# Optimization experiments

Hardware: AMD Instinct MI355X
Metric: run time of the kernel (lower is better)

## Reference

```python
import jax, jax.numpy as jnp
import numpy as np


def gcn_conv(x, edge_index, edge_weight, W, b):
    """PyG-style GCNConv: h = x @ W; add self-loops (w=1); sym deg^-1/2 norm;
    scatter-add aggregation; + bias."""
    N = x.shape[0]
    h = x @ W                                   # [N, F_out]
    row, col = edge_index[0], edge_index[1]     # src, dst
    loop = jnp.arange(N)
    row = jnp.concatenate([row, loop])
    col = jnp.concatenate([col, loop])
    ew = jnp.concatenate([edge_weight, jnp.ones((N,), edge_weight.dtype)])
    deg = jax.ops.segment_sum(ew, col, num_segments=N)
    dinv = jnp.where(deg > 0, deg ** -0.5, 0.0)
    norm = dinv[row] * ew * dinv[col]           # [E+N]
    out = jax.ops.segment_sum(h[row] * norm[:, None], col, num_segments=N)
    return out + b


def setup_inputs() -> dict:
    key = jax.random.key(0)
    ks = jax.random.split(key, 12)
    N, F_in, H, O, E = 20000, 3000, 512, 256, 640000
    x = jax.random.normal(ks[0], (N, F_in), dtype=jnp.float32)
    sim_edge_index = jax.random.randint(ks[1], (2, E), 0, N, dtype=jnp.int64)
    sim_edge_weight = jax.random.uniform(ks[2], (E,), dtype=jnp.float32)
    dist_edge_index = jax.random.randint(ks[3], (2, E), 0, N, dtype=jnp.int64)
    dist_edge_weight = jax.random.uniform(ks[4], (E,), dtype=jnp.float32)
    s = 0.02
    return {
        "x": x,
        "sim_edge_index": sim_edge_index,
        "sim_edge_weight": sim_edge_weight,
        "dist_edge_index": dist_edge_index,
        "dist_edge_weight": dist_edge_weight,
        "W1": jax.random.normal(ks[5], (F_in, H), dtype=jnp.float32) * s,
        "b1": jnp.zeros((H,), jnp.float32),
        "W2": jax.random.normal(ks[6], (F_in, H), dtype=jnp.float32) * s,
        "b2": jnp.zeros((H,), jnp.float32),
        "Ws": jax.random.normal(ks[7], (H, O), dtype=jnp.float32) * s,
        "bs": jnp.zeros((O,), jnp.float32),
        "Wd": jax.random.normal(ks[8], (H, O), dtype=jnp.float32) * s,
        "bd": jnp.zeros((O,), jnp.float32),
        "Wf": jax.random.normal(ks[9], (2 * O, O), dtype=jnp.float32) * s,
        "bf": jnp.zeros((O,), jnp.float32),
    }


def reference(x, sim_edge_index, sim_edge_weight, dist_edge_index,
              dist_edge_weight, W1, b1, W2, b2, Ws, bs, Wd, bd, Wf, bf):
    # eval mode: dropout is identity
    xs = jax.nn.relu(gcn_conv(x, sim_edge_index, sim_edge_weight, W1, b1))
    xd = jax.nn.relu(gcn_conv(x, dist_edge_index, dist_edge_weight, W2, b2))
    x_sim = gcn_conv(xs, sim_edge_index, sim_edge_weight, Ws, bs)
    x_dist = gcn_conv(xd, dist_edge_index, dist_edge_weight, Wd, bd)
    fused = jnp.concatenate([x_sim, x_dist], axis=1) @ Wf + bf
    return (x_sim, x_dist, fused)
```

## Files before the change

kernel.cpp:

```cpp
#include <hip/hip_runtime.h>
#include <cstdint>
#include <cstddef>

typedef unsigned short u16;
typedef __bf16 bf16x8 __attribute__((ext_vector_type(8)));
typedef float f32x4 __attribute__((ext_vector_type(4)));

#define N_NODES 20000
#define MPAD    20096
#define E_EDGES 640000
#define K1      3000
#define K1P     3008
#define H_DIM   512
#define NW      1024
#define O_DIM   256

__device__ __forceinline__ float bf2f(unsigned int hi) {
  union { unsigned int u; float f; } v; v.u = hi << 16; return v.f;
}
__device__ __forceinline__ u16 f2bf(float f) {
  union { float f; unsigned int u; } v; v.f = f;
  unsigned int u = v.u;
  return (u16)((u + 0x7fffu + ((u >> 16) & 1u)) >> 16);
}

__device__ __forceinline__ void gl2lds16(const void* g, void* l) {
  __builtin_amdgcn_global_load_lds((const __attribute__((address_space(1))) void*)g,
                                   (__attribute__((address_space(3))) void*)l, 16, 0, 0);
}

__global__ __launch_bounds__(256) void deg_init_k(float* degS, float* degD, int* cntS, int* cntD) {
  int i = blockIdx.x * 256 + threadIdx.x;
  if (i < N_NODES) { degS[i] = 1.0f; degD[i] = 1.0f; cntS[i] = 0; cntD[i] = 0; }
}

__global__ __launch_bounds__(256) void deg_accum_k(const int* eiS, const float* ewS,
                                                   const int* eiD, const float* ewD,
                                                   float* degS, float* degD, int* cntS, int* cntD) {
  int e = blockIdx.x * 256 + threadIdx.x;
  if (e < E_EDGES) {
    int cs = eiS[E_EDGES + e];
    atomicAdd(&degS[cs], ewS[e]);
    atomicAdd(&cntS[cs], 1);
    int cd = eiD[E_EDGES + e];
    atomicAdd(&degD[cd], ewD[e]);
    atomicAdd(&cntD[cd], 1);
  }
}

__global__ __launch_bounds__(256) void dinv_k(const float* degS, const float* degD,
                                              float* dinvS, float* dinvD) {
  int i = blockIdx.x * 256 + threadIdx.x;
  if (i < N_NODES) { dinvS[i] = rsqrtf(degS[i]); dinvD[i] = rsqrtf(degD[i]); }
}

__global__ __launch_bounds__(1024) void scan_k(const int* cntS, int* offS, int* curS,
                                               const int* cntD, int* offD, int* curD) {
  const int* cnt = blockIdx.x ? cntD : cntS;
  int* off = blockIdx.x ? offD : offS;
  int* cur = blockIdx.x ? curD : curS;
  __shared__ int sums[1024];
  const int t = threadIdx.x;
  const int CH = 20;
  int base = t * CH;
  int s = 0;
  for (int j = 0; j < CH; ++j) { int idx = base + j; if (idx < N_NODES) s += cnt[idx]; }
  sums[t] = s;
  __syncthreads();
  for (int d = 1; d < 1024; d <<= 1) {
    int v = (t >= d) ? sums[t - d] : 0;
    __syncthreads();
    sums[t] += v;
    __syncthreads();
  }
  int run = sums[t] - s;
  for (int j = 0; j < CH; ++j) {
    int idx = base + j;
    if (idx <= N_NODES) {
      off[idx] = run; cur[idx] = run;
      if (idx < N_NODES) run += cnt[idx];
    }
  }
}

__global__ __launch_bounds__(256) void scatter_k(const int* eiS, const float* ewS, const float* dinvS,
                                                 int* curS, int* ssrcS, float* snrmS,
                                                 const int* eiD, const float* ewD, const float* dinvD,
                                                 int* curD, int* ssrcD, float* snrmD) {
  int e = blockIdx.x * 256 + threadIdx.x;
  if (e < E_EDGES) {
    {
      int r = eiS[e], c = eiS[E_EDGES + e];
      int pos = atomicAdd(&curS[c], 1);
      ssrcS[pos] = r;
      snrmS[pos] = dinvS[r] * ewS[e] * dinvS[c];
    }
    {
      int r = eiD[e], c = eiD[E_EDGES + e];
      int pos = atomicAdd(&curD[c], 1);
      ssrcD[pos] = r;
      snrmD[pos] = dinvD[r] * ewD[e] * dinvD[c];
    }
  }
}

__global__ __launch_bounds__(256) void conv_x_k(const float* __restrict__ x, u16* __restrict__ xb) {
  const int row = blockIdx.x;
  for (int c = threadIdx.x; c < 376; c += 256) {
    uint4 o = {0, 0, 0, 0};
    if (row < N_NODES && c < 375) {
      const float4* p = (const float4*)(x + (size_t)row * K1 + (size_t)c * 8);
      float4 v0 = p[0], v1 = p[1];
      o.x = f2bf(v0.x) | ((unsigned)f2bf(v0.y) << 16);
      o.y = f2bf(v0.z) | ((unsigned)f2bf(v0.w) << 16);
      o.z = f2bf(v1.x) | ((unsigned)f2bf(v1.y) << 16);
      o.w = f2bf(v1.z) | ((unsigned)f2bf(v1.w) << 16);
    }
    *(uint4*)(xb + (size_t)row * K1P + (size_t)c * 8) = o;
  }
}

__global__ __launch_bounds__(256) void conv_w12_k(const float* __restrict__ W1,
                                                  const float* __restrict__ W2,
                                                  u16* __restrict__ w12t) {
  __shared__ float t[64][65];
  const int kb = blockIdx.x;
  const int nb = blockIdx.y;
  const int n0 = nb * 64;
  const float* W = (n0 < H_DIM) ? W1 : W2;
  const int nn0 = n0 & (H_DIM - 1);
  const int k0 = kb * 64;
  const int tc = threadIdx.x & 63;
  const int tr4 = threadIdx.x >> 6;
#pragma unroll
  for (int rr = 0; rr < 16; ++rr) {
    int r = tr4 * 16 + rr;
    int k = k0 + r;
    t[r][tc] = (k < K1) ? W[(size_t)k * H_DIM + nn0 + tc] : 0.f;
  }
  __syncthreads();
#pragma unroll
  for (int rr = 0; rr < 16; ++rr) {
    int n = tr4 * 16 + rr;
    w12t[(size_t)(n0 + n) * K1P + k0 + tc] = f2bf(t[tc][n]);
  }
}

__global__ __launch_bounds__(256) void conv_wsm_k(const float* Ws, const float* Wd, const float* Wf,
                                                  u16* wst, u16* wdt, u16* wft) {
  __shared__ float t[64][65];
  const int which = blockIdx.z;
  const float* W = (which == 0) ? Ws : (which == 1) ? Wd : Wf;
  u16* o = (which == 0) ? wst : (which == 1) ? wdt : wft;
  const int k0 = blockIdx.x * 64;
  const int n0 = blockIdx.y * 64;
  const int tc = threadIdx.x & 63;
  const int tr4 = threadIdx.x >> 6;
#pragma unroll
  for (int rr = 0; rr < 16; ++rr) {
    int r = tr4 * 16 + rr;
    t[r][tc] = W[(size_t)(k0 + r) * O_DIM + n0 + tc];
  }
  __syncthreads();
#pragma unroll
  for (int rr = 0; rr < 16; ++rr) {
    int n = tr4 * 16 + rr;
    o[(size_t)(n0 + n) * H_DIM + k0 + tc] = f2bf(t[tc][n]);
  }
}

template <typename CT, bool BIAS>
__device__ __forceinline__ void gemm_body(const u16* __restrict__ A, const u16* __restrict__ Bt,
                                          CT* __restrict__ C, const float* __restrict__ bias,
                                          int Mreal, int K, int ldc, int bm, int bn) {
  __shared__ alignas(16) u16 As[128 * 64];
  __shared__ alignas(16) u16 Bs[128 * 64];
  const int tid = threadIdx.x;
  const int lane = tid & 63;
  const int wv = tid >> 6;

  const int wm = (wv >> 1) << 6;
  const int wn = (wv & 1) << 6;
  const int frow = lane & 15;
  const int q = lane >> 4;
  const int r7 = lane & 7;

  const int srow = tid >> 3;
  const int sgr = ((tid & 7) ^ ((tid >> 3) & 7)) << 3;
  const u16* ga = A + (size_t)(bm + srow) * K + sgr;
  const u16* gb = Bt + (size_t)(bn + srow) * K + sgr;
  u16* la = &As[wv * 512];
  u16* lb = &Bs[wv * 512];

  f32x4 acc[4][4] = {};

  for (int k0 = 0; k0 < K; k0 += 64) {
#pragma unroll
    for (int r = 0; r < 4; ++r) {
      gl2lds16(ga + (size_t)(r * 32) * K + k0, la + r * 2048);
      gl2lds16(gb + (size_t)(r * 32) * K + k0, lb + r * 2048);
    }
    __syncthreads();
#pragma unroll
    for (int ks = 0; ks < 64; ks += 32) {
      const int p = (((q + (ks >> 3)) ^ r7) << 3);
      bf16x8 af[4], bv[4];
#pragma unroll
      for (int t = 0; t < 4; ++t) {
        af[t] = *(const bf16x8*)&As[(wm + t * 16 + frow) * 64 + p];
        bv[t] = *(const bf16x8*)&Bs[(wn + t * 16 + frow) * 64 + p];
      }
#pragma unroll
      for (int i = 0; i < 4; ++i)
#pragma unroll
        for (int j = 0; j < 4; ++j)
          acc[i][j] = __builtin_amdgcn_mfma_f32_16x16x32_bf16(af[i], bv[j], acc[i][j], 0, 0, 0);
    }
    __syncthreads();
  }

  const int crow = (lane >> 4) << 2;
  const int ccol = lane & 15;
#pragma unroll
  for (int i = 0; i < 4; ++i) {
#pragma unroll
    for (int r = 0; r < 4; ++r) {
      int gr = bm + wm + i * 16 + crow + r;
      if (gr < Mreal) {
#pragma unroll
        for (int j = 0; j < 4; ++j) {
          int gc = bn + wn + j * 16 + ccol;
          float v = acc[i][j][r];
          if constexpr (BIAS) v += bias[gc];
          if constexpr (sizeof(CT) == 2) C[(size_t)gr * ldc + gc] = (CT)f2bf(v);
          else C[(size_t)gr * ldc + gc] = (CT)v;
        }
      }
    }
  }
}

__global__ __launch_bounds__(256) void gemm_big_k(const u16* __restrict__ A,
                                                  const u16* __restrict__ Bt,
                                                  u16* __restrict__ C) {
  const int h = blockIdx.y * 8 + blockIdx.x;
  const int chunk = 157;
  const int L = (h & 7) * chunk + (h >> 3);
  const int bn = (L & 7) * 128;
  const int bm = (L >> 3) * 128;
  gemm_body<u16, false>(A, Bt, C, nullptr, N_NODES, K1P, NW, bm, bn);
}

__global__ __launch_bounds__(256) void gemm_pair_k(const u16* A0, const u16* B0, u16* C0,
                                                   const u16* A1, const u16* B1, u16* C1) {
  const u16* A = blockIdx.z ? A1 : A0;
  const u16* Bt = blockIdx.z ? B1 : B0;
  u16* C = blockIdx.z ? C1 : C0;
  gemm_body<u16, false>(A, Bt, C, nullptr, N_NODES, H_DIM, O_DIM,
                        blockIdx.y * 128, blockIdx.x * 128);
}

__global__ __launch_bounds__(256) void gemm_f_k(const u16* A, const u16* Bt, float* C,
                                                const float* bias) {
  gemm_body<float, true>(A, Bt, C, bias, N_NODES, H_DIM, O_DIM,
                         blockIdx.y * 128, blockIdx.x * 128);
}

__global__ __launch_bounds__(256) void agg1_k(const u16* __restrict__ h12,
                                              const int* offS, const int* srcS, const float* nrmS,
                                              const float* dinvS, const float* b1,
                                              const int* offD, const int* srcD, const float* nrmD,
                                              const float* dinvD, const float* b2,
                                              u16* __restrict__ xsd) {
  const int lane = threadIdx.x & 63;
  const int wv = threadIdx.x >> 6;
  const int i = blockIdx.x * 4 + wv;
  const int g = blockIdx.y;
  if (i >= MPAD) return;
  u16* outp = xsd + ((size_t)g * MPAD + i) * H_DIM + lane * 8;
  if (i >= N_NODES) { uint4 z = {0, 0, 0, 0}; *(uint4*)outp = z; return; }

  const int* off = g ? offD : offS;
  const int* src = g ? srcD : srcS;
  const float* nrm = g ? nrmD : nrmS;
  const float* dinv = g ? dinvD : dinvS;
  const float* bias = g ? b2 : b1;
  const u16* hb = h12 + (size_t)g * H_DIM + lane * 8;

  float a[8];
  float dv = dinv[i];
  float sw = dv * dv;
  uint4 u = *(const uint4*)(hb + (size_t)i * NW);
  a[0] = sw * bf2f(u.x & 0xffff); a[1] = sw * bf2f(u.x >> 16);
  a[2] = sw * bf2f(u.y & 0xffff); a[3] = sw * bf2f(u.y >> 16);
  a[4] = sw * bf2f(u.z & 0xffff); a[5] = sw * bf2f(u.z >> 16);
  a[6] = sw * bf2f(u.w & 0xffff); a[7] = sw * bf2f(u.w >> 16);

  const int e0 = off[i], e1 = off[i + 1];
  int e = e0;
  for (; e + 4 <= e1; e += 4) {
    int ss[4]; float ww[4];
#pragma unroll
    for (int t = 0; t < 4; ++t) { ss[t] = src[e + t]; ww[t] = nrm[e + t]; }
    uint4 vv[4];
#pragma unroll
    for (int t = 0; t < 4; ++t) vv[t] = *(const uint4*)(hb + (size_t)ss[t] * NW);
#pragma unroll
    for (int t = 0; t < 4; ++t) {
      float w = ww[t]; uint4 v = vv[t];
      a[0] += w * bf2f(v.x & 0xffff); a[1] += w * bf2f(v.x >> 16);
      a[2] += w * bf2f(v.y & 0xffff); a[3] += w * bf2f(v.y >> 16);
      a[4] += w * bf2f(v.z & 0xffff); a[5] += w * bf2f(v.z >> 16);
      a[6] += w * bf2f(v.w & 0xffff); a[7] += w * bf2f(v.w >> 16);
    }
  }
  for (; e < e1; ++e) {
    int s = src[e];
    float w = nrm[e];
    uint4 v = *(const uint4*)(hb + (size_t)s * NW);
    a[0] += w * bf2f(v.x & 0xffff); a[1] += w * bf2f(v.x >> 16);
    a[2] += w * bf2f(v.y & 0xffff); a[3] += w * bf2f(v.y >> 16);
    a[4] += w * bf2f(v.z & 0xffff); a[5] += w * bf2f(v.z >> 16);
    a[6] += w * bf2f(v.w & 0xffff); a[7] += w * bf2f(v.w >> 16);
  }
  float4 bA = *(const float4*)(bias + lane * 8);
  float4 bB = *(const float4*)(bias + lane * 8 + 4);
  a[0] = fmaxf(a[0] + bA.x, 0.f); a[1] = fmaxf(a[1] + bA.y, 0.f);
  a[2] = fmaxf(a[2] + bA.z, 0.f); a[3] = fmaxf(a[3] + bA.w, 0.f);
  a[4] = fmaxf(a[4] + bB.x, 0.f); a[5] = fmaxf(a[5] + bB.y, 0.f);
  a[6] = fmaxf(a[6] + bB.z, 0.f); a[7] = fmaxf(a[7] + bB.w, 0.f);
  uint4 o;
  o.x = f2bf(a[0]) | ((unsigned)f2bf(a[1]) << 16);
  o.y = f2bf(a[2]) | ((unsigned)f2bf(a[3]) << 16);
  o.z = f2bf(a[4]) | ((unsigned)f2bf(a[5]) << 16);
  o.w = f2bf(a[6]) | ((unsigned)f2bf(a[7]) << 16);
  *(uint4*)outp = o;
}

__global__ __launch_bounds__(256) void agg2_k(const u16* __restrict__ hsb, const u16* __restrict__ hdb,
                                              const int* offS, const int* srcS, const float* nrmS,
                                              const float* dinvS, const float* bs,
                                              const int* offD, const int* srcD, const float* nrmD,
                                              const float* dinvD, const float* bd,
                                              float* __restrict__ outF, u16* __restrict__ xcat) {
  const int lane = threadIdx.x & 63;
  const int wv = threadIdx.x >> 6;
  const int i = blockIdx.x * 4 + wv;
  const int g = blockIdx.y;
  if (i >= MPAD) return;
  u16* oc = xcat + (size_t)i * H_DIM + (size_t)g * O_DIM + lane * 4;
  if (i >= N_NODES) { uint2 z = {0, 0}; *(uint2*)oc = z; return; }

  const u16* h = g ? hdb : hsb;
  const int* off = g ? offD : offS;
  const int* src = g ? srcD : srcS;
  const float* nrm = g ? nrmD : nrmS;
  const float* dinv = g ? dinvD : dinvS;
  const float* bias = g ? bd : bs;
  const u16* hb = h + lane * 4;

  float a[4];
  float dv = dinv[i];
  float sw = dv * dv;
  uint2 u = *(const uint2*)(hb + (size_t)i * O_DIM);
  a[0] = sw * bf2f(u.x & 0xffff); a[1] = sw * bf2f(u.x >> 16);
  a[2] = sw * bf2f(u.y & 0xffff); a[3] = sw * bf2f(u.y >> 16);

  const int e0 = off[i], e1 = off[i + 1];
  int e = e0;
  for (; e + 8 <= e1; e += 8) {
    int ss[8]; float ww[8];
#pragma unroll
    for (int t = 0; t < 8; ++t) { ss[t] = src[e + t]; ww[t] = nrm[e + t]; }
    uint2 vv[8];
#pragma unroll
    for (int t = 0; t < 8; ++t) vv[t] = *(const uint2*)(hb + (size_t)ss[t] * O_DIM);
#pragma unroll
    for (int t = 0; t < 8; ++t) {
      float w = ww[t]; uint2 v = vv[t];
      a[0] += w * bf2f(v.x & 0xffff); a[1] += w * bf2f(v.x >> 16);
      a[2] += w * bf2f(v.y & 0xffff); a[3] += w * bf2f(v.y >> 16);
    }
  }
  for (; e < e1; ++e) {
    int s = src[e];
    float w = nrm[e];
    uint2 v = *(const uint2*)(hb + (size_t)s * O_DIM);
    a[0] += w * bf2f(v.x & 0xffff); a[1] += w * bf2f(v.x >> 16);
    a[2] += w * bf2f(v.y & 0xffff); a[3] += w * bf2f(v.y >> 16);
  }
  float4 bb = *(const float4*)(bias + lane * 4);
  a[0] += bb.x; a[1] += bb.y; a[2] += bb.z; a[3] += bb.w;

  float4 fo = {a[0], a[1], a[2], a[3]};
  *(float4*)(outF + (size_t)g * N_NODES * O_DIM + (size_t)i * O_DIM + lane * 4) = fo;
  uint2 o;
  o.x = f2bf(a[0]) | ((unsigned)f2bf(a[1]) << 16);
  o.y = f2bf(a[2]) | ((unsigned)f2bf(a[3]) << 16);
  *(uint2*)oc = o;
}

extern "C" void kernel_launch(void* const* d_in, const int* in_sizes, int n_in,
                              void* d_out, int out_size, void* d_ws, size_t ws_size,
                              hipStream_t stream) {
  const float* x = (const float*)d_in[0];
  const int* eiS = (const int*)d_in[1];
  const float* ewS = (const float*)d_in[2];
  const int* eiD = (const int*)d_in[3];
  const float* ewD = (const float*)d_in[4];
  const float* W1 = (const float*)d_in[5];
  const float* b1 = (const float*)d_in[6];
  const float* W2 = (const float*)d_in[7];
  const float* b2 = (const float*)d_in[8];
  const float* Ws = (const float*)d_in[9];
  const float* bs = (const float*)d_in[10];
  const float* Wd = (const float*)d_in[11];
  const float* bd = (const float*)d_in[12];
  const float* Wf = (const float*)d_in[13];
  const float* bf_ = (const float*)d_in[14];
  float* out = (float*)d_out;

  char* p = (char*)d_ws;
  auto alloc = [&](size_t n) -> char* { char* r = p; p += (n + 255) & ~(size_t)255; return r; };

  u16* xb    = (u16*)alloc((size_t)MPAD * K1P * 2);
  u16* w12t  = (u16*)alloc((size_t)NW * K1P * 2);
  u16* h12   = (u16*)alloc((size_t)N_NODES * NW * 2);
  u16* xsd   = (u16*)alloc((size_t)2 * MPAD * H_DIM * 2);
  u16* hsb   = (u16*)alloc((size_t)N_NODES * O_DIM * 2);
  u16* hdb   = (u16*)alloc((size_t)N_NODES * O_DIM * 2);
  u16* xcat  = (u16*)alloc((size_t)MPAD * H_DIM * 2);
  u16* wst   = (u16*)alloc((size_t)O_DIM * H_DIM * 2);
  u16* wdt   = (u16*)alloc((size_t)O_DIM * H_DIM * 2);
  u16* wft   = (u16*)alloc((size_t)O_DIM * H_DIM * 2);
  float* degS = (float*)alloc((size_t)N_NODES * 4);
  float* degD = (float*)alloc((size_t)N_NODES * 4);
  float* dinvS = (float*)alloc((size_t)N_NODES * 4);
  float* dinvD = (float*)alloc((size_t)N_NODES * 4);
  int* cntS = (int*)alloc((size_t)N_NODES * 4);
  int* cntD = (int*)alloc((size_t)N_NODES * 4);
  int* offS = (int*)alloc((size_t)(N_NODES + 1) * 4);
  int* offD = (int*)alloc((size_t)(N_NODES + 1) * 4);
  int* curS = (int*)alloc((size_t)(N_NODES + 1) * 4);
  int* curD = (int*)alloc((size_t)(N_NODES + 1) * 4);
  int* ssrcS = (int*)alloc((size_t)E_EDGES * 4);
  int* ssrcD = (int*)alloc((size_t)E_EDGES * 4);
  float* snrmS = (float*)alloc((size_t)E_EDGES * 4);
  float* snrmD = (float*)alloc((size_t)E_EDGES * 4);

  const int gN = (N_NODES + 255) / 256;
  const int gE = (E_EDGES + 255) / 256;

  deg_init_k<<<gN, 256, 0, stream>>>(degS, degD, cntS, cntD);
  deg_accum_k<<<gE, 256, 0, stream>>>(eiS, ewS, eiD, ewD, degS, degD, cntS, cntD);
  dinv_k<<<gN, 256, 0, stream>>>(degS, degD, dinvS, dinvD);
  scan_k<<<2, 1024, 0, stream>>>(cntS, offS, curS, cntD, offD, curD);
  scatter_k<<<gE, 256, 0, stream>>>(eiS, ewS, dinvS, curS, ssrcS, snrmS,
                                    eiD, ewD, dinvD, curD, ssrcD, snrmD);

  conv_x_k<<<MPAD, 256, 0, stream>>>(x, xb);
  conv_w12_k<<<dim3(47, 16), 256, 0, stream>>>(W1, W2, w12t);
  conv_wsm_k<<<dim3(8, 4, 3), 256, 0, stream>>>(Ws, Wd, Wf, wst, wdt, wft);

  gemm_big_k<<<dim3(8, 157), 256, 0, stream>>>(xb, w12t, h12);

  agg1_k<<<dim3(MPAD / 4, 2), 256, 0, stream>>>(h12, offS, ssrcS, snrmS, dinvS, b1,
                                                offD, ssrcD, snrmD, dinvD, b2, xsd);

  gemm_pair_k<<<dim3(2, 157, 2), 256, 0, stream>>>(xsd, wst, hsb,
                                                   xsd + (size_t)MPAD * H_DIM, wdt, hdb);

  agg2_k<<<dim3(MPAD / 4, 2), 256, 0, stream>>>(hsb, hdb, offS, ssrcS, snrmS, dinvS, bs,
                                                offD, ssrcD, snrmD, dinvD, bd, out, xcat);

  gemm_f_k<<<dim3(2, 157), 256, 0, stream>>>(xcat, wft, out + (size_t)2 * N_NODES * O_DIM, bf_);
}
```

Before: 1.052 ms.

## Record per-edge slot in degree pass, fuse dinv into scan, unroll gather by six

The degree-counting pass now saves the return value of each count atomic as the edge's slot within its destination bucket. The scatter pass then computes its position as offset plus slot and no longer needs a second round of atomics. The dinv kernel is folded into the scan kernel, which stages counts in LDS and writes offsets in coalesced form, removing one launch and a cursor array. The first aggregation loop is unrolled from 4 to 6 edges to keep more gathers in flight. In exchange it adds two edge-sized buffers and more register pressure.

```diff
diff --git a/kernel.cpp b/kernel.cpp
--- a/kernel.cpp
+++ b/kernel.cpp
@@ -36,35 +36,43 @@
 
 __global__ __launch_bounds__(256) void deg_accum_k(const int* eiS, const float* ewS,
                                                    const int* eiD, const float* ewD,
-                                                   float* degS, float* degD, int* cntS, int* cntD) {
+                                                   float* degS, float* degD, int* cntS, int* cntD,
+                                                   int* eposS, int* eposD) {
   int e = blockIdx.x * 256 + threadIdx.x;
   if (e < E_EDGES) {
     int cs = eiS[E_EDGES + e];
     atomicAdd(&degS[cs], ewS[e]);
-    atomicAdd(&cntS[cs], 1);
+    eposS[e] = atomicAdd(&cntS[cs], 1);
     int cd = eiD[E_EDGES + e];
     atomicAdd(&degD[cd], ewD[e]);
-    atomicAdd(&cntD[cd], 1);
-  }
-}
-
-__global__ __launch_bounds__(256) void dinv_k(const float* degS, const float* degD,
-                                              float* dinvS, float* dinvD) {
-  int i = blockIdx.x * 256 + threadIdx.x;
-  if (i < N_NODES) { dinvS[i] = rsqrtf(degS[i]); dinvD[i] = rsqrtf(degD[i]); }
-}
-
-__global__ __launch_bounds__(1024) void scan_k(const int* cntS, int* offS, int* curS,
-                                               const int* cntD, int* offD, int* curD) {
+    eposD[e] = atomicAdd(&cntD[cd], 1);
+  }
+}
+
+__global__ __launch_bounds__(1024) void scan_k(const int* cntS, int* offS,
+                                               const float* degS, float* dinvS,
+                                               const int* cntD, int* offD,
+                                               const float* degD, float* dinvD) {
+  extern __shared__ int lds[];
+  int* sums = lds;
+  int* lcnt = lds + 1024;
   const int* cnt = blockIdx.x ? cntD : cntS;
   int* off = blockIdx.x ? offD : offS;
-  int* cur = blockIdx.x ? curD : curS;
-  __shared__ int sums[1024];
+  const float* deg = blockIdx.x ? degD : degS;
+  float* dinv = blockIdx.x ? dinvD : dinvS;
   const int t = threadIdx.x;
+
+  for (int idx = t; idx < N_NODES; idx += 1024) {
+    lcnt[idx] = cnt[idx];
+    dinv[idx] = rsqrtf(deg[idx]);
+  }
+  __syncthreads();
+
   const int CH = 20;
-  int base = t * CH;
+  const int base = t * CH;
   int s = 0;
-  for (int j = 0; j < CH; ++j) { int idx = base + j; if (idx < N_NODES) s += cnt[idx]; }
+#pragma unroll
+  for (int j = 0; j < CH; ++j) { int idx = base + j; if (idx < N_NODES) s += lcnt[idx]; }
   sums[t] = s;
   __syncthreads();
   for (int d = 1; d < 1024; d <<= 1) {
@@ -74,30 +82,33 @@
     __syncthreads();
   }
   int run = sums[t] - s;
+#pragma unroll
   for (int j = 0; j < CH; ++j) {
     int idx = base + j;
-    if (idx <= N_NODES) {
-      off[idx] = run; cur[idx] = run;
-      if (idx < N_NODES) run += cnt[idx];
-    }
-  }
+    if (idx < N_NODES) { int c = lcnt[idx]; lcnt[idx] = run; run += c; }
+  }
+  __syncthreads();
+  for (int idx = t; idx < N_NODES; idx += 1024) off[idx] = lcnt[idx];
+  if (t == 1023) off[N_NODES] = run;
 }
 
 __global__ __launch_bounds__(256) void scatter_k(const int* eiS, const float* ewS, const float* dinvS,
-                                                 int* curS, int* ssrcS, float* snrmS,
+                                                 const int* offS, const int* eposS,
+                                                 int* ssrcS, float* snrmS,
                                                  const int* eiD, const float* ewD, const float* dinvD,
-                                                 int* curD, int* ssrcD, float* snrmD) {
+                                                 const int* offD, const int* eposD,
+                                                 int* ssrcD, float* snrmD) {
   int e = blockIdx.x * 256 + threadIdx.x;
   if (e < E_EDGES) {
     {
       int r = eiS[e], c = eiS[E_EDGES + e];
-      int pos = atomicAdd(&curS[c], 1);
+      int pos = offS[c] + eposS[e];
       ssrcS[pos] = r;
       snrmS[pos] = dinvS[r] * ewS[e] * dinvS[c];
     }
     {
       int r = eiD[e], c = eiD[E_EDGES + e];
-      int pos = atomicAdd(&curD[c], 1);
+      int pos = offD[c] + eposD[e];
       ssrcD[pos] = r;
       snrmD[pos] = dinvD[r] * ewD[e] * dinvD[c];
     }
@@ -298,15 +309,15 @@
 
   const int e0 = off[i], e1 = off[i + 1];
   int e = e0;
-  for (; e + 4 <= e1; e += 4) {
-    int ss[4]; float ww[4];
-#pragma unroll
-    for (int t = 0; t < 4; ++t) { ss[t] = src[e + t]; ww[t] = nrm[e + t]; }
-    uint4 vv[4];
-#pragma unroll
-    for (int t = 0; t < 4; ++t) vv[t] = *(const uint4*)(hb + (size_t)ss[t] * NW);
-#pragma unroll
-    for (int t = 0; t < 4; ++t) {
+  for (; e + 6 <= e1; e += 6) {
+    int ss[6]; float ww[6];
+#pragma unroll
+    for (int t = 0; t < 6; ++t) { ss[t] = src[e + t]; ww[t] = nrm[e + t]; }
+    uint4 vv[6];
+#pragma unroll
+    for (int t = 0; t < 6; ++t) vv[t] = *(const uint4*)(hb + (size_t)ss[t] * NW);
+#pragma unroll
+    for (int t = 0; t < 6; ++t) {
       float w = ww[t]; uint4 v = vv[t];
       a[0] += w * bf2f(v.x & 0xffff); a[1] += w * bf2f(v.x >> 16);
       a[2] += w * bf2f(v.y & 0xffff); a[3] += w * bf2f(v.y >> 16);
@@ -441,8 +452,8 @@
   int* cntD = (int*)alloc((size_t)N_NODES * 4);
   int* offS = (int*)alloc((size_t)(N_NODES + 1) * 4);
   int* offD = (int*)alloc((size_t)(N_NODES + 1) * 4);
-  int* curS = (int*)alloc((size_t)(N_NODES + 1) * 4);
-  int* curD = (int*)alloc((size_t)(N_NODES + 1) * 4);
+  int* eposS = (int*)alloc((size_t)E_EDGES * 4);
+  int* eposD = (int*)alloc((size_t)E_EDGES * 4);
   int* ssrcS = (int*)alloc((size_t)E_EDGES * 4);
   int* ssrcD = (int*)alloc((size_t)E_EDGES * 4);
   float* snrmS = (float*)alloc((size_t)E_EDGES * 4);
@@ -452,11 +463,11 @@
   const int gE = (E_EDGES + 255) / 256;
 
   deg_init_k<<<gN, 256, 0, stream>>>(degS, degD, cntS, cntD);
-  deg_accum_k<<<gE, 256, 0, stream>>>(eiS, ewS, eiD, ewD, degS, degD, cntS, cntD);
-  dinv_k<<<gN, 256, 0, stream>>>(degS, degD, dinvS, dinvD);
-  scan_k<<<2, 1024, 0, stream>>>(cntS, offS, curS, cntD, offD, curD);
-  scatter_k<<<gE, 256, 0, stream>>>(eiS, ewS, dinvS, curS, ssrcS, snrmS,
-                                    eiD, ewD, dinvD, curD, ssrcD, snrmD);
+  deg_accum_k<<<gE, 256, 0, stream>>>(eiS, ewS, eiD, ewD, degS, degD, cntS, cntD, eposS, eposD);
+  scan_k<<<2, 1024, (size_t)(1024 + N_NODES) * 4, stream>>>(cntS, offS, degS, dinvS,
+                                                            cntD, offD, degD, dinvD);
+  scatter_k<<<gE, 256, 0, stream>>>(eiS, ewS, dinvS, offS, eposS, ssrcS, snrmS,
+                                    eiD, ewD, dinvD, offD, eposD, ssrcD, snrmD);
 
   conv_x_k<<<MPAD, 256, 0, stream>>>(x, xb);
   conv_w12_k<<<dim3(47, 16), 256, 0, stream>>>(W1, W2, w12t);
```

Measured after the change: 1.022 ms. -2.8%, faster.
